# Kernel optimization log

Hardware: AMD Instinct MI355X
Metric: run time of the kernel (lower is better)

The kernel has to match this reference:

```python
import jax, jax.numpy as jnp
import numpy as np

N_NODES = 50000
N_EDGES = 1250000
IN_CH, HID_CH, OUT_CH = 128, 64, 10
N_GRAPHS = 500


def gcn_conv(x, W, src, dst, n_nodes):
    # GCNConv (bias=False, normalize=True, add_self_loops=True):
    # out = D^{-1/2} (A + I) D^{-1/2} X W
    h = x @ W  # [N, H]
    loop = jnp.arange(n_nodes, dtype=src.dtype)
    s = jnp.concatenate([src, loop])
    d = jnp.concatenate([dst, loop])
    deg = jax.ops.segment_sum(jnp.ones_like(d, dtype=h.dtype), d, num_segments=n_nodes)
    dinv = jnp.where(deg > 0, jax.lax.rsqrt(deg), 0.0)
    norm = dinv[s] * dinv[d]  # [E+N]
    msgs = h[s] * norm[:, None]  # gather + normalize
    return jax.ops.segment_sum(msgs, d, num_segments=n_nodes)  # scatter-add


def setup_inputs() -> dict:
    key = jax.random.key(0)
    ks = jax.random.split(key, 8)
    x = jax.random.normal(ks[0], (N_NODES, IN_CH), dtype=jnp.float32)
    edge_index = jax.random.randint(ks[1], (2, N_EDGES), 0, N_NODES, dtype=jnp.int64)
    batch = jnp.sort(jax.random.randint(ks[2], (N_NODES,), 0, N_GRAPHS, dtype=jnp.int64))
    def glorot(k, fan_in, fan_out):
        lim = np.sqrt(6.0 / (fan_in + fan_out))
        return jax.random.uniform(k, (fan_in, fan_out), jnp.float32, -lim, lim)
    W1 = glorot(ks[3], IN_CH, HID_CH)
    W2 = glorot(ks[4], HID_CH, HID_CH)
    W3 = glorot(ks[5], HID_CH, HID_CH)
    Wl = glorot(ks[6], HID_CH, OUT_CH)
    bl = jnp.zeros((OUT_CH,), jnp.float32)
    return {"x": x, "edge_index": edge_index, "batch": batch,
            "W1": W1, "W2": W2, "W3": W3, "Wl": Wl, "bl": bl}


def reference(x, edge_index, batch, W1, W2, W3, Wl, bl):
    src, dst = edge_index[0], edge_index[1]
    n = x.shape[0]
    h = jax.nn.relu(gcn_conv(x, W1, src, dst, n))
    h = jax.nn.relu(gcn_conv(h, W2, src, dst, n))
    h = gcn_conv(h, W3, src, dst, n)
    # global_mean_pool over graph ids
    sums = jax.ops.segment_sum(h, batch, num_segments=N_GRAPHS)
    cnts = jax.ops.segment_sum(jnp.ones((n,), h.dtype), batch, num_segments=N_GRAPHS)
    pooled = sums / jnp.maximum(cnts, 1.0)[:, None]
    return pooled @ Wl + bl
```

## Files before the change

kernel.cpp:

```cpp
#include <hip/hip_runtime.h>

#define CH 64
#define CHUNK 4096
#define BSHIFT 8
#define NBUCK 196

__device__ __forceinline__ unsigned short f2bf_rne(float f) {
    unsigned int u = __float_as_uint(f);
    u += 0x7fffu + ((u >> 16) & 1u);
    return (unsigned short)(u >> 16);
}
__device__ __forceinline__ float bf_lo(unsigned int q) {
    return __uint_as_float(q << 16);
}
__device__ __forceinline__ float bf_hi(unsigned int q) {
    return __uint_as_float(q & 0xffff0000u);
}
__device__ __forceinline__ unsigned int pack2bf(float lo, float hi) {
    return (unsigned int)f2bf_rne(lo) | ((unsigned int)f2bf_rne(hi) << 16);
}

template <int K>
__global__ __launch_bounds__(256) void gemm1_hist_kernel(
        const float* __restrict__ X, const float* __restrict__ W,
        unsigned short* __restrict__ G, int N,
        const int* __restrict__ dst, int* __restrict__ bucket_cnt, int E,
        int gemm_blocks) {
    constexpr int KC  = 64;
    constexpr int XLD = KC + 4;
    __shared__ float Xs[64 * XLD];
    __shared__ float Wls[KC * CH];
    __shared__ int hist[256];
    int tid = threadIdx.x;

    if (blockIdx.x >= gemm_blocks) {
        int cid = blockIdx.x - gemm_blocks;
        int e0 = cid * CHUNK;
        int total = min(CHUNK, E - e0);
        hist[tid] = 0;
        __syncthreads();
        for (int i = tid; i < total; i += 256)
            atomicAdd(&hist[dst[e0 + i] >> BSHIFT], 1);
        __syncthreads();
        if (tid < NBUCK && hist[tid]) atomicAdd(&bucket_cnt[tid], hist[tid]);
        return;
    }

    int tx  = tid & 15;
    int ty  = tid >> 4;
    int row_tile = blockIdx.x * 64;
    int r0 = ty * 4;
    float acc[4][4] = {{0.f}};

    for (int kc = 0; kc < K; kc += KC) {
        __syncthreads();
#pragma unroll
        for (int t = 0; t < 4; ++t) {
            int idx = tid + t * 256;
            int row = idx >> 4;
            int k4  = idx & 15;
            int grow = row_tile + row;
            const float4* xs = (const float4*)(X + (size_t)min(grow, N - 1) * K + kc);
            *(float4*)&Xs[row * XLD + 4 * k4] = xs[k4];
        }
#pragma unroll
        for (int t = 0; t < 4; ++t) {
            int idx = tid + t * 256;
            *(float4*)&Wls[idx * 4] = ((const float4*)(W + (size_t)kc * CH))[idx];
        }
        __syncthreads();
#pragma unroll
        for (int kk = 0; kk < KC; kk += 4) {
            float xr[4][4], wr[4][4];
#pragma unroll
            for (int i = 0; i < 4; ++i) {
                float4 v = *(const float4*)&Xs[(r0 + i) * XLD + kk];
                xr[i][0] = v.x; xr[i][1] = v.y; xr[i][2] = v.z; xr[i][3] = v.w;
            }
#pragma unroll
            for (int j = 0; j < 4; ++j) {
                float4 v = *(const float4*)&Wls[(kk + j) * CH + 4 * tx];
                wr[j][0] = v.x; wr[j][1] = v.y; wr[j][2] = v.z; wr[j][3] = v.w;
            }
#pragma unroll
            for (int i = 0; i < 4; ++i)
#pragma unroll
                for (int j = 0; j < 4; ++j)
#pragma unroll
                    for (int c = 0; c < 4; ++c)
                        acc[i][c] = fmaf(xr[i][j], wr[j][c], acc[i][c]);
        }
    }
#pragma unroll
    for (int i = 0; i < 4; ++i) {
        int r = row_tile + r0 + i;
        if (r < N) {
            ushort4 o;
            o.x = f2bf_rne(acc[i][0]);
            o.y = f2bf_rne(acc[i][1]);
            o.z = f2bf_rne(acc[i][2]);
            o.w = f2bf_rne(acc[i][3]);
            ((ushort4*)G)[(size_t)r * 16 + tx] = o;
        }
    }
}

__global__ __launch_bounds__(256) void scan_gptr_kernel(
        const int* __restrict__ cnt,
        int* __restrict__ bucket_base, int* __restrict__ cursor,
        int* __restrict__ rowptr,
        const int* __restrict__ batch, int* __restrict__ gptr,
        int N, int E, int NG) {
    if (blockIdx.x == 0) {
        __shared__ int sc[256];
        int t = threadIdx.x;
        int c = (t < NBUCK) ? cnt[t] : 0;
        sc[t] = c;
        __syncthreads();
        for (int off = 1; off < 256; off <<= 1) {
            int v = (t >= off) ? sc[t - off] : 0;
            __syncthreads();
            sc[t] += v;
            __syncthreads();
        }
        if (t < NBUCK) { bucket_base[t] = sc[t] - c; cursor[t] = sc[t] - c; }
        if (t == NBUCK - 1) bucket_base[NBUCK] = sc[t];
        if (t == 0) rowptr[N] = E;
    } else {
        for (int g = threadIdx.x; g <= NG; g += 256) {
            if (g == NG) { gptr[NG] = N; continue; }
            int lo = 0, hi = N;
            while (lo < hi) {
                int mid = (lo + hi) >> 1;
                if (batch[mid] < g) lo = mid + 1; else hi = mid;
            }
            gptr[g] = lo;
        }
    }
}

__global__ __launch_bounds__(256) void bin_kernel(
        const int* __restrict__ src, const int* __restrict__ dst,
        int* __restrict__ cursor, unsigned int* __restrict__ pairs, int E) {
    __shared__ unsigned int stage[CHUNK];
    __shared__ int hist[256], sc[256], lbase[256], lcur[256], gbase[256];
    int tid = threadIdx.x;
    int e0 = blockIdx.x * CHUNK;
    int total = min(CHUNK, E - e0);
    hist[tid] = 0;
    __syncthreads();
    for (int i = tid; i < total; i += 256)
        atomicAdd(&hist[dst[e0 + i] >> BSHIFT], 1);
    __syncthreads();
    sc[tid] = hist[tid];
    __syncthreads();
    for (int off = 1; off < 256; off <<= 1) {
        int v = (tid >= off) ? sc[tid - off] : 0;
        __syncthreads();
        sc[tid] += v;
        __syncthreads();
    }
    lbase[tid] = sc[tid] - hist[tid];
    lcur[tid]  = sc[tid] - hist[tid];
    if (tid < NBUCK && hist[tid] > 0) gbase[tid] = atomicAdd(&cursor[tid], hist[tid]);
    __syncthreads();
    for (int i = tid; i < total; i += 256) {
        unsigned int s = (unsigned int)src[e0 + i];
        unsigned int d = (unsigned int)dst[e0 + i];
        int pos = atomicAdd(&lcur[d >> BSHIFT], 1);
        stage[pos] = (d << 16) | s;
    }
    __syncthreads();
    for (int i = tid; i < total; i += 256) {
        unsigned int p = stage[i];
        int b = (int)(p >> 24);
        pairs[gbase[b] + (i - lbase[b])] = p;
    }
}

__global__ __launch_bounds__(256) void bucket_sort_kernel(
        const unsigned int* __restrict__ pairs, const int* __restrict__ base,
        unsigned short* __restrict__ csr, int* __restrict__ rowptr,
        float* __restrict__ dinv, int N) {
    __shared__ int cntl[256], sc[256], cur[256];
    int tid = threadIdx.x;
    int b = blockIdx.x;
    int pbase = base[b], pend = base[b + 1];
    int cnt = pend - pbase;
    cntl[tid] = 0;
    __syncthreads();
    for (int i = tid; i < cnt; i += 256)
        atomicAdd(&cntl[(pairs[pbase + i] >> 16) & 255u], 1);
    __syncthreads();
    sc[tid] = cntl[tid];
    __syncthreads();
    for (int off = 1; off < 256; off <<= 1) {
        int v = (tid >= off) ? sc[tid - off] : 0;
        __syncthreads();
        sc[tid] += v;
        __syncthreads();
    }
    int excl = sc[tid] - cntl[tid];
    cur[tid] = excl;
    int v = (b << BSHIFT) + tid;
    if (v < N) {
        rowptr[v] = pbase + excl;
        dinv[v] = rsqrtf((float)(cntl[tid] + 1));
    }
    __syncthreads();
    for (int i = tid; i < cnt; i += 256) {
        unsigned int p = pairs[pbase + i];
        int pos = atomicAdd(&cur[(p >> 16) & 255u], 1);
        csr[pbase + pos] = (unsigned short)(p & 0xffffu);
    }
}

template <bool PRESCALED, bool F32OUT>
__global__ __launch_bounds__(256) void aggregate_kernel(
        const unsigned short* __restrict__ G, const int* __restrict__ rowptr,
        const unsigned short* __restrict__ csr, const float* __restrict__ dinv,
        void* __restrict__ Out, int N, int E, int relu) {
    int lane = threadIdx.x & 63;
    int w = (blockIdx.x * 256 + threadIdx.x) >> 6;
    int grp = lane >> 3, cl = lane & 7;
    int v = w * 8 + grp;
    bool valid = v < N;
    int vc = valid ? v : N - 1;
    int beg = rowptr[vc];
    int cnt = valid ? rowptr[vc + 1] - beg : 0;
    int mx = cnt;
    mx = max(mx, __shfl_xor(mx, 8));
    mx = max(mx, __shfl_xor(mx, 16));
    mx = max(mx, __shfl_xor(mx, 32));

    const uint4* __restrict__ G4 = (const uint4*)G;
    float a0 = 0.f, a1 = 0.f, a2 = 0.f, a3 = 0.f;
    float a4 = 0.f, a5 = 0.f, a6 = 0.f, a7 = 0.f;
    float b0 = 0.f, b1 = 0.f, b2 = 0.f, b3 = 0.f;
    float b4 = 0.f, b5 = 0.f, b6 = 0.f, b7 = 0.f;
    int nit = (mx + 1) >> 1;
#pragma unroll 2
    for (int it = 0; it < nit; ++it) {
        int i0 = 2 * it, i1 = i0 + 1;
        int e0 = min(beg + i0, E - 1);
        int e1 = min(beg + i1, E - 1);
        bool ok0 = i0 < cnt, ok1 = i1 < cnt;
        int u0 = ok0 ? (int)csr[e0] : 0;
        int u1 = ok1 ? (int)csr[e1] : 0;
        float s0, s1;
        if (PRESCALED) { s0 = ok0 ? 1.f : 0.f;        s1 = ok1 ? 1.f : 0.f; }
        else           { s0 = ok0 ? dinv[u0] : 0.f;   s1 = ok1 ? dinv[u1] : 0.f; }
        uint4 q0 = G4[(size_t)u0 * 8 + cl];
        uint4 q1 = G4[(size_t)u1 * 8 + cl];
        a0 = fmaf(bf_lo(q0.x), s0, a0); a1 = fmaf(bf_hi(q0.x), s0, a1);
        a2 = fmaf(bf_lo(q0.y), s0, a2); a3 = fmaf(bf_hi(q0.y), s0, a3);
        a4 = fmaf(bf_lo(q0.z), s0, a4); a5 = fmaf(bf_hi(q0.z), s0, a5);
        a6 = fmaf(bf_lo(q0.w), s0, a6); a7 = fmaf(bf_hi(q0.w), s0, a7);
        b0 = fmaf(bf_lo(q1.x), s1, b0); b1 = fmaf(bf_hi(q1.x), s1, b1);
        b2 = fmaf(bf_lo(q1.y), s1, b2); b3 = fmaf(bf_hi(q1.y), s1, b3);
        b4 = fmaf(bf_lo(q1.z), s1, b4); b5 = fmaf(bf_hi(q1.z), s1, b5);
        b6 = fmaf(bf_lo(q1.w), s1, b6); b7 = fmaf(bf_hi(q1.w), s1, b7);
    }
    a0 += b0; a1 += b1; a2 += b2; a3 += b3;
    a4 += b4; a5 += b5; a6 += b6; a7 += b7;
    if (valid) {
        uint4 q = G4[(size_t)v * 8 + cl];
        float d = dinv[v];
        float sv = PRESCALED ? 1.f : d;
        float o0 = (a0 + bf_lo(q.x) * sv) * d, o1 = (a1 + bf_hi(q.x) * sv) * d;
        float o2 = (a2 + bf_lo(q.y) * sv) * d, o3 = (a3 + bf_hi(q.y) * sv) * d;
        float o4 = (a4 + bf_lo(q.z) * sv) * d, o5 = (a5 + bf_hi(q.z) * sv) * d;
        float o6 = (a6 + bf_lo(q.w) * sv) * d, o7 = (a7 + bf_hi(q.w) * sv) * d;
        if (relu) {
            o0 = fmaxf(o0, 0.f); o1 = fmaxf(o1, 0.f); o2 = fmaxf(o2, 0.f);
            o3 = fmaxf(o3, 0.f); o4 = fmaxf(o4, 0.f); o5 = fmaxf(o5, 0.f);
            o6 = fmaxf(o6, 0.f); o7 = fmaxf(o7, 0.f);
        }
        if (F32OUT) {
            float4 w0 = {o0, o1, o2, o3}, w1 = {o4, o5, o6, o7};
            ((float4*)Out)[(size_t)v * 16 + cl * 2]     = w0;
            ((float4*)Out)[(size_t)v * 16 + cl * 2 + 1] = w1;
        } else {
            uint4 p;
            p.x = pack2bf(o0, o1); p.y = pack2bf(o2, o3);
            p.z = pack2bf(o4, o5); p.w = pack2bf(o6, o7);
            ((uint4*)Out)[(size_t)v * 8 + cl] = p;
        }
    }
}

__global__ __launch_bounds__(256) void gemm_bf16_kernel(
        const unsigned short* __restrict__ Xbf, const float* __restrict__ W,
        const float* __restrict__ dinv, unsigned short* __restrict__ G, int N) {
    constexpr int XLDU = 36;
    __shared__ unsigned int Xs[64 * XLDU];
    __shared__ float Wls[64 * CH];
    int tid = threadIdx.x;
    int tx  = tid & 15;
    int ty  = tid >> 4;
    int row_tile = blockIdx.x * 64;
    int r0 = ty * 4;
    float acc[4][4] = {{0.f}};

#pragma unroll
    for (int t = 0; t < 2; ++t) {
        int idx = tid + t * 256;
        int row = idx >> 3;
        int k4  = idx & 7;
        int grow = row_tile + row;
        uint4 v = ((const uint4*)Xbf)[(size_t)min(grow, N - 1) * 8 + k4];
        *(uint4*)&Xs[row * XLDU + 4 * k4] = v;
    }
#pragma unroll
    for (int t = 0; t < 4; ++t) {
        int idx = tid + t * 256;
        *(float4*)&Wls[idx * 4] = ((const float4*)W)[idx];
    }
    __syncthreads();
#pragma unroll
    for (int kk = 0; kk < 64; kk += 4) {
        float xr[4][4], wr[4][4];
#pragma unroll
        for (int i = 0; i < 4; ++i) {
            uint2 q = *(const uint2*)&Xs[(r0 + i) * XLDU + (kk >> 1)];
            xr[i][0] = bf_lo(q.x); xr[i][1] = bf_hi(q.x);
            xr[i][2] = bf_lo(q.y); xr[i][3] = bf_hi(q.y);
        }
#pragma unroll
        for (int j = 0; j < 4; ++j) {
            float4 v = *(const float4*)&Wls[(kk + j) * CH + 4 * tx];
            wr[j][0] = v.x; wr[j][1] = v.y; wr[j][2] = v.z; wr[j][3] = v.w;
        }
#pragma unroll
        for (int i = 0; i < 4; ++i)
#pragma unroll
            for (int j = 0; j < 4; ++j)
#pragma unroll
                for (int c = 0; c < 4; ++c)
                    acc[i][c] = fmaf(xr[i][j], wr[j][c], acc[i][c]);
    }
#pragma unroll
    for (int i = 0; i < 4; ++i) {
        int r = row_tile + r0 + i;
        if (r < N) {
            float d = dinv[r];
            ushort4 o;
            o.x = f2bf_rne(acc[i][0] * d);
            o.y = f2bf_rne(acc[i][1] * d);
            o.z = f2bf_rne(acc[i][2] * d);
            o.w = f2bf_rne(acc[i][3] * d);
            ((ushort4*)G)[(size_t)r * 16 + tx] = o;
        }
    }
}

__global__ __launch_bounds__(64) void pool_head_kernel(
        const float* __restrict__ H, const int* __restrict__ gptr,
        const float* __restrict__ Wl, const float* __restrict__ bl,
        float* __restrict__ out, int NG) {
    int g = blockIdx.x;
    int lane = threadIdx.x;
    int s = gptr[g], e = gptr[g + 1];
    float acc = 0.f;
    for (int v = s; v < e; ++v) acc += H[(size_t)v * CH + lane];
    float c = (float)(e - s);
    float mean = (c > 0.f) ? acc / c : 0.f;
    for (int o = 0; o < 10; ++o) {
        float t = mean * Wl[lane * 10 + o];
        for (int off = 32; off > 0; off >>= 1) t += __shfl_down(t, off);
        if (lane == 0) out[g * 10 + o] = t + bl[o];
    }
}

extern "C" void kernel_launch(void* const* d_in, const int* in_sizes, int n_in,
                              void* d_out, int out_size, void* d_ws, size_t ws_size,
                              hipStream_t stream) {
    const float* x     = (const float*)d_in[0];
    const int*   ei    = (const int*)d_in[1];
    const int*   batch = (const int*)d_in[2];
    const float* W1    = (const float*)d_in[3];
    const float* W2    = (const float*)d_in[4];
    const float* W3    = (const float*)d_in[5];
    const float* Wl    = (const float*)d_in[6];
    const float* bl    = (const float*)d_in[7];
    float* out = (float*)d_out;

    const int N  = in_sizes[0] / 128;
    const int E  = in_sizes[1] / 2;
    const int NG = out_size / 10;

    const int* src = ei;
    const int* dst = ei + E;

    const int cb = (E + CHUNK - 1) / CHUNK;

    char* ws = (char*)d_ws;
    size_t off = 0;
    auto alloc = [&](size_t bytes) -> void* {
        void* p = ws + off;
        off += bytes;
        off = (off + 255) & ~(size_t)255;
        return p;
    };
    int*   bucket_cnt  = (int*)alloc((size_t)NBUCK * 4);
    int*   bucket_base = (int*)alloc((size_t)(NBUCK + 1) * 4);
    int*   cursor      = (int*)alloc((size_t)NBUCK * 4);
    unsigned short* csr = (unsigned short*)alloc((size_t)(E + 64) * 2);
    int*   rowptr = (int*)alloc((size_t)(N + 1) * 4);
    float* dinv   = (float*)alloc((size_t)N * 4);
    int*   gptrb  = (int*)alloc((size_t)(NG + 1) * 4);
    unsigned short* GA = (unsigned short*)alloc((size_t)N * CH * 2);
    unsigned short* GB = (unsigned short*)alloc((size_t)N * CH * 2);
    float* hbuf   = (float*)alloc((size_t)N * CH * 4);
    unsigned int* pairs = (unsigned int*)hbuf;

    hipMemsetAsync(bucket_cnt, 0, (size_t)NBUCK * 4, stream);

    int gb = (N + 63) / 64;
    int ab = ((N + 7) / 8 + 3) / 4;

    gemm1_hist_kernel<128><<<gb + cb, 256, 0, stream>>>(x, W1, GA, N,
                                                        dst, bucket_cnt, E, gb);
    scan_gptr_kernel<<<2, 256, 0, stream>>>(bucket_cnt, bucket_base, cursor,
                                            rowptr, batch, gptrb, N, E, NG);
    bin_kernel<<<cb, 256, 0, stream>>>(src, dst, cursor, pairs, E);
    bucket_sort_kernel<<<NBUCK, 256, 0, stream>>>(pairs, bucket_base, csr, rowptr, dinv, N);

    aggregate_kernel<false, false><<<ab, 256, 0, stream>>>(GA, rowptr, csr, dinv,
                                                           GB, N, E, 1);
    gemm_bf16_kernel<<<gb, 256, 0, stream>>>(GB, W2, dinv, GA, N);
    aggregate_kernel<true, false><<<ab, 256, 0, stream>>>(GA, rowptr, csr, dinv,
                                                          GB, N, E, 1);
    gemm_bf16_kernel<<<gb, 256, 0, stream>>>(GB, W3, dinv, GA, N);
    aggregate_kernel<true, true><<<ab, 256, 0, stream>>>(GA, rowptr, csr, dinv,
                                                         hbuf, N, E, 0);

    pool_head_kernel<<<NG, 64, 0, stream>>>(hbuf, gptrb, Wl, bl, out, NG);
}
```

Before: 238.7 us.

## Fuse first GEMM with edge binning and store final layer output as bf16

Moves the first-layer GEMM out of the histogram kernel and into the binning kernel, so the GEMM blocks run alongside the heavier binning work rather than the light histogram pass. The binning staging arrays reuse the GEMM shared-memory buffers. The last aggregation now writes bf16 into GB instead of fp32 into a separate buffer, and the pooling kernel reads bf16, which halves that traffic. In exchange, the final-layer output loses precision, and the pairs buffer now aliases GB.

```diff
diff --git a/kernel.cpp b/kernel.cpp
--- a/kernel.cpp
+++ b/kernel.cpp
@@ -20,89 +20,18 @@
     return (unsigned int)f2bf_rne(lo) | ((unsigned int)f2bf_rne(hi) << 16);
 }
 
-template <int K>
-__global__ __launch_bounds__(256) void gemm1_hist_kernel(
-        const float* __restrict__ X, const float* __restrict__ W,
-        unsigned short* __restrict__ G, int N,
-        const int* __restrict__ dst, int* __restrict__ bucket_cnt, int E,
-        int gemm_blocks) {
-    constexpr int KC  = 64;
-    constexpr int XLD = KC + 4;
-    __shared__ float Xs[64 * XLD];
-    __shared__ float Wls[KC * CH];
+__global__ __launch_bounds__(256) void hist_kernel(
+        const int* __restrict__ dst, int* __restrict__ bucket_cnt, int E) {
     __shared__ int hist[256];
     int tid = threadIdx.x;
-
-    if (blockIdx.x >= gemm_blocks) {
-        int cid = blockIdx.x - gemm_blocks;
-        int e0 = cid * CHUNK;
-        int total = min(CHUNK, E - e0);
-        hist[tid] = 0;
-        __syncthreads();
-        for (int i = tid; i < total; i += 256)
-            atomicAdd(&hist[dst[e0 + i] >> BSHIFT], 1);
-        __syncthreads();
-        if (tid < NBUCK && hist[tid]) atomicAdd(&bucket_cnt[tid], hist[tid]);
-        return;
-    }
-
-    int tx  = tid & 15;
-    int ty  = tid >> 4;
-    int row_tile = blockIdx.x * 64;
-    int r0 = ty * 4;
-    float acc[4][4] = {{0.f}};
-
-    for (int kc = 0; kc < K; kc += KC) {
-        __syncthreads();
-#pragma unroll
-        for (int t = 0; t < 4; ++t) {
-            int idx = tid + t * 256;
-            int row = idx >> 4;
-            int k4  = idx & 15;
-            int grow = row_tile + row;
-            const float4* xs = (const float4*)(X + (size_t)min(grow, N - 1) * K + kc);
-            *(float4*)&Xs[row * XLD + 4 * k4] = xs[k4];
-        }
-#pragma unroll
-        for (int t = 0; t < 4; ++t) {
-            int idx = tid + t * 256;
-            *(float4*)&Wls[idx * 4] = ((const float4*)(W + (size_t)kc * CH))[idx];
-        }
-        __syncthreads();
-#pragma unroll
-        for (int kk = 0; kk < KC; kk += 4) {
-            float xr[4][4], wr[4][4];
-#pragma unroll
-            for (int i = 0; i < 4; ++i) {
-                float4 v = *(const float4*)&Xs[(r0 + i) * XLD + kk];
-                xr[i][0] = v.x; xr[i][1] = v.y; xr[i][2] = v.z; xr[i][3] = v.w;
-            }
-#pragma unroll
-            for (int j = 0; j < 4; ++j) {
-                float4 v = *(const float4*)&Wls[(kk + j) * CH + 4 * tx];
-                wr[j][0] = v.x; wr[j][1] = v.y; wr[j][2] = v.z; wr[j][3] = v.w;
-            }
-#pragma unroll
-            for (int i = 0; i < 4; ++i)
-#pragma unroll
-                for (int j = 0; j < 4; ++j)
-#pragma unroll
-                    for (int c = 0; c < 4; ++c)
-                        acc[i][c] = fmaf(xr[i][j], wr[j][c], acc[i][c]);
-        }
-    }
-#pragma unroll
-    for (int i = 0; i < 4; ++i) {
-        int r = row_tile + r0 + i;
-        if (r < N) {
-            ushort4 o;
-            o.x = f2bf_rne(acc[i][0]);
-            o.y = f2bf_rne(acc[i][1]);
-            o.z = f2bf_rne(acc[i][2]);
-            o.w = f2bf_rne(acc[i][3]);
-            ((ushort4*)G)[(size_t)r * 16 + tx] = o;
-        }
-    }
+    int e0 = blockIdx.x * CHUNK;
+    int total = min(CHUNK, E - e0);
+    hist[tid] = 0;
+    __syncthreads();
+    for (int i = tid; i < total; i += 256)
+        atomicAdd(&hist[dst[e0 + i] >> BSHIFT], 1);
+    __syncthreads();
+    if (tid < NBUCK && hist[tid]) atomicAdd(&bucket_cnt[tid], hist[tid]);
 }
 
 __global__ __launch_bounds__(256) void scan_gptr_kernel(
@@ -139,42 +68,117 @@
     }
 }
 
-__global__ __launch_bounds__(256) void bin_kernel(
+template <int K>
+__global__ __launch_bounds__(256) void gemm1_bin_kernel(
+        const float* __restrict__ X, const float* __restrict__ W,
+        unsigned short* __restrict__ G, int N,
         const int* __restrict__ src, const int* __restrict__ dst,
-        int* __restrict__ cursor, unsigned int* __restrict__ pairs, int E) {
-    __shared__ unsigned int stage[CHUNK];
-    __shared__ int hist[256], sc[256], lbase[256], lcur[256], gbase[256];
+        int* __restrict__ cursor, unsigned int* __restrict__ pairs, int E,
+        int gemm_blocks) {
+    constexpr int KC  = 64;
+    constexpr int XLD = KC + 4;
+    __shared__ float Xs[64 * XLD];
+    __shared__ float Wls[KC * CH];
     int tid = threadIdx.x;
-    int e0 = blockIdx.x * CHUNK;
-    int total = min(CHUNK, E - e0);
-    hist[tid] = 0;
-    __syncthreads();
-    for (int i = tid; i < total; i += 256)
-        atomicAdd(&hist[dst[e0 + i] >> BSHIFT], 1);
-    __syncthreads();
-    sc[tid] = hist[tid];
-    __syncthreads();
-    for (int off = 1; off < 256; off <<= 1) {
-        int v = (tid >= off) ? sc[tid - off] : 0;
-        __syncthreads();
-        sc[tid] += v;
-        __syncthreads();
-    }
-    lbase[tid] = sc[tid] - hist[tid];
-    lcur[tid]  = sc[tid] - hist[tid];
-    if (tid < NBUCK && hist[tid] > 0) gbase[tid] = atomicAdd(&cursor[tid], hist[tid]);
-    __syncthreads();
-    for (int i = tid; i < total; i += 256) {
-        unsigned int s = (unsigned int)src[e0 + i];
-        unsigned int d = (unsigned int)dst[e0 + i];
-        int pos = atomicAdd(&lcur[d >> BSHIFT], 1);
-        stage[pos] = (d << 16) | s;
-    }
-    __syncthreads();
-    for (int i = tid; i < total; i += 256) {
-        unsigned int p = stage[i];
-        int b = (int)(p >> 24);
-        pairs[gbase[b] + (i - lbase[b])] = p;
+
+    if (blockIdx.x >= gemm_blocks) {
+        unsigned int* stage = (unsigned int*)Xs;
+        int* hist  = (int*)Wls;
+        int* sc    = hist + 256;
+        int* lbase = hist + 512;
+        int* lcur  = hist + 768;
+        int* gbase = hist + 1024;
+        int cid = blockIdx.x - gemm_blocks;
+        int e0 = cid * CHUNK;
+        int total = min(CHUNK, E - e0);
+        hist[tid] = 0;
+        __syncthreads();
+        for (int i = tid; i < total; i += 256)
+            atomicAdd(&hist[dst[e0 + i] >> BSHIFT], 1);
+        __syncthreads();
+        sc[tid] = hist[tid];
+        __syncthreads();
+        for (int off = 1; off < 256; off <<= 1) {
+            int v = (tid >= off) ? sc[tid - off] : 0;
+            __syncthreads();
+            sc[tid] += v;
+            __syncthreads();
+        }
+        lbase[tid] = sc[tid] - hist[tid];
+        lcur[tid]  = sc[tid] - hist[tid];
+        if (tid < NBUCK && hist[tid] > 0) gbase[tid] = atomicAdd(&cursor[tid], hist[tid]);
+        __syncthreads();
+        for (int i = tid; i < total; i += 256) {
+            unsigned int s = (unsigned int)src[e0 + i];
+            unsigned int d = (unsigned int)dst[e0 + i];
+            int pos = atomicAdd(&lcur[d >> BSHIFT], 1);
+            stage[pos] = (d << 16) | s;
+        }
+        __syncthreads();
+        for (int i = tid; i < total; i += 256) {
+            unsigned int p = stage[i];
+            int b = (int)(p >> 24);
+            pairs[gbase[b] + (i - lbase[b])] = p;
+        }
+        return;
+    }
+
+    int tx  = tid & 15;
+    int ty  = tid >> 4;
+    int row_tile = blockIdx.x * 64;
+    int r0 = ty * 4;
+    float acc[4][4] = {{0.f}};
+
+    for (int kc = 0; kc < K; kc += KC) {
+        __syncthreads();
+#pragma unroll
+        for (int t = 0; t < 4; ++t) {
+            int idx = tid + t * 256;
+            int row = idx >> 4;
+            int k4  = idx & 15;
+            int grow = row_tile + row;
+            const float4* xs = (const float4*)(X + (size_t)min(grow, N - 1) * K + kc);
+            *(float4*)&Xs[row * XLD + 4 * k4] = xs[k4];
+        }
+#pragma unroll
+        for (int t = 0; t < 4; ++t) {
+            int idx = tid + t * 256;
+            *(float4*)&Wls[idx * 4] = ((const float4*)(W + (size_t)kc * CH))[idx];
+        }
+        __syncthreads();
+#pragma unroll
+        for (int kk = 0; kk < KC; kk += 4) {
+            float xr[4][4], wr[4][4];
+#pragma unroll
+            for (int i = 0; i < 4; ++i) {
+                float4 v = *(const float4*)&Xs[(r0 + i) * XLD + kk];
+                xr[i][0] = v.x; xr[i][1] = v.y; xr[i][2] = v.z; xr[i][3] = v.w;
+            }
+#pragma unroll
+            for (int j = 0; j < 4; ++j) {
+                float4 v = *(const float4*)&Wls[(kk + j) * CH + 4 * tx];
+                wr[j][0] = v.x; wr[j][1] = v.y; wr[j][2] = v.z; wr[j][3] = v.w;
+            }
+#pragma unroll
+            for (int i = 0; i < 4; ++i)
+#pragma unroll
+                for (int j = 0; j < 4; ++j)
+#pragma unroll
+                    for (int c = 0; c < 4; ++c)
+                        acc[i][c] = fmaf(xr[i][j], wr[j][c], acc[i][c]);
+        }
+    }
+#pragma unroll
+    for (int i = 0; i < 4; ++i) {
+        int r = row_tile + r0 + i;
+        if (r < N) {
+            ushort4 o;
+            o.x = f2bf_rne(acc[i][0]);
+            o.y = f2bf_rne(acc[i][1]);
+            o.z = f2bf_rne(acc[i][2]);
+            o.w = f2bf_rne(acc[i][3]);
+            ((ushort4*)G)[(size_t)r * 16 + tx] = o;
+        }
     }
 }
 
@@ -355,14 +359,17 @@
 }
 
 __global__ __launch_bounds__(64) void pool_head_kernel(
-        const float* __restrict__ H, const int* __restrict__ gptr,
+        const unsigned short* __restrict__ H, const int* __restrict__ gptr,
         const float* __restrict__ Wl, const float* __restrict__ bl,
         float* __restrict__ out, int NG) {
     int g = blockIdx.x;
     int lane = threadIdx.x;
     int s = gptr[g], e = gptr[g + 1];
     float acc = 0.f;
-    for (int v = s; v < e; ++v) acc += H[(size_t)v * CH + lane];
+    for (int v = s; v < e; ++v) {
+        unsigned int u = (unsigned int)H[(size_t)v * CH + lane];
+        acc += __uint_as_float(u << 16);
+    }
     float c = (float)(e - s);
     float mean = (c > 0.f) ? acc / c : 0.f;
     for (int o = 0; o < 10; ++o) {
@@ -411,19 +418,18 @@
     int*   gptrb  = (int*)alloc((size_t)(NG + 1) * 4);
     unsigned short* GA = (unsigned short*)alloc((size_t)N * CH * 2);
     unsigned short* GB = (unsigned short*)alloc((size_t)N * CH * 2);
-    float* hbuf   = (float*)alloc((size_t)N * CH * 4);
-    unsigned int* pairs = (unsigned int*)hbuf;
+    unsigned int* pairs = (unsigned int*)GB;
 
     hipMemsetAsync(bucket_cnt, 0, (size_t)NBUCK * 4, stream);
 
     int gb = (N + 63) / 64;
     int ab = ((N + 7) / 8 + 3) / 4;
 
-    gemm1_hist_kernel<128><<<gb + cb, 256, 0, stream>>>(x, W1, GA, N,
-                                                        dst, bucket_cnt, E, gb);
+    hist_kernel<<<cb, 256, 0, stream>>>(dst, bucket_cnt, E);
     scan_gptr_kernel<<<2, 256, 0, stream>>>(bucket_cnt, bucket_base, cursor,
                                             rowptr, batch, gptrb, N, E, NG);
-    bin_kernel<<<cb, 256, 0, stream>>>(src, dst, cursor, pairs, E);
+    gemm1_bin_kernel<128><<<gb + cb, 256, 0, stream>>>(x, W1, GA, N,
+                                                       src, dst, cursor, pairs, E, gb);
     bucket_sort_kernel<<<NBUCK, 256, 0, stream>>>(pairs, bucket_base, csr, rowptr, dinv, N);
 
     aggregate_kernel<false, false><<<ab, 256, 0, stream>>>(GA, rowptr, csr, dinv,
@@ -432,8 +438,8 @@
     aggregate_kernel<true, false><<<ab, 256, 0, stream>>>(GA, rowptr, csr, dinv,
                                                           GB, N, E, 1);
     gemm_bf16_kernel<<<gb, 256, 0, stream>>>(GB, W3, dinv, GA, N);
-    aggregate_kernel<true, true><<<ab, 256, 0, stream>>>(GA, rowptr, csr, dinv,
-                                                         hbuf, N, E, 0);
-
-    pool_head_kernel<<<NG, 64, 0, stream>>>(hbuf, gptrb, Wl, bl, out, NG);
-}
+    aggregate_kernel<true, false><<<ab, 256, 0, stream>>>(GA, rowptr, csr, dinv,
+                                                          GB, N, E, 0);
+
+    pool_head_kernel<<<NG, 64, 0, stream>>>(GB, gptrb, Wl, bl, out, NG);
+}
```

After: 238.2 us. Within noise of the previous version (-0.2%).
